# Optimization experiments

Measured on AMD Instinct MI355X. Metric: run time of the kernel, lower is better.

The kernel has to match this reference:

```python
import jax, jax.numpy as jnp
import numpy as np

ALPHA = 0.2  # LeakyReLU negative slope
NEG_INF = -9e15


def setup_inputs() -> dict:
    key = jax.random.key(0)
    k1, k2, k3, k4 = jax.random.split(key, 4)
    B, N, Fin, Fout = 4, 4096, 256, 128
    h = jax.random.normal(k1, (B, N, Fin), dtype=jnp.float32)
    adj = jax.random.randint(k2, (B, N, N), 0, 2, dtype=jnp.int32)  # {0,1} adjacency
    # xavier_uniform with gain 1.414
    limW = 1.414 * np.sqrt(6.0 / (Fin + Fout))
    W = jax.random.uniform(k3, (Fin, Fout), jnp.float32, -limW, limW)
    lima = 1.414 * np.sqrt(6.0 / (2 * Fout + 1))
    a = jax.random.uniform(k4, (2 * Fout, 1), jnp.float32, -lima, lima)
    return {"h": h, "adj": adj, "W": W, "a": a}


def reference(h, adj, W, a):
    # Wh: [B, N, Fout]
    Wh = jnp.einsum('bni,io->bno', h, W)
    Fout = W.shape[1]
    # Decompose a^T [Wh_i || Wh_j] = a1.Wh_i + a2.Wh_j (identical math, avoids
    # materializing the [B,N,N,2F] concat tensor the torch code builds).
    a1, a2 = a[:Fout, 0], a[Fout:, 0]
    s1 = jnp.einsum('bno,o->bn', Wh, a1)  # [B, N]
    s2 = jnp.einsum('bno,o->bn', Wh, a2)  # [B, N]
    e = jax.nn.leaky_relu(s1[:, :, None] + s2[:, None, :], negative_slope=ALPHA)  # [B,N,N]
    attention = jnp.where(adj > 0, e, jnp.asarray(NEG_INF, e.dtype))
    attention = jax.nn.softmax(attention, axis=2)
    # dropout is inactive in eval mode (training=False)
    # Faithful to the torch code: the FIRST h_prime is overwritten; the output is
    # einsum('bjk,bji->bki', attention, Wh) -> sums over the softmax (row) axis j.
    h_prime = jnp.einsum('bjk,bji->bki', attention, Wh)  # [B, N, Fout]
    return jax.nn.elu(h_prime)  # concat=True
```

## Files before the change

kernel.cpp:

```cpp
#include <hip/hip_runtime.h>
#include <hip/hip_bf16.h>

#define ALPHA 0.2f
#define L2E 1.4426950408889634f

constexpr int Nn = 4096;
constexpr int FIN = 256;
constexpr int FOUT = 128;
constexpr int JC = 4;
constexpr int JQ = 1024;
constexpr int NCH = 32;
constexpr long long SLAB = 2097152;

typedef __attribute__((ext_vector_type(8))) short short8;
typedef __attribute__((ext_vector_type(8))) unsigned short ushort8;
typedef __attribute__((ext_vector_type(4))) float f32x4;
typedef __attribute__((ext_vector_type(16))) float f32x16;
typedef __attribute__((ext_vector_type(4))) int int4v;

__device__ __forceinline__ unsigned short f2bf(float x) {
  unsigned int u = __float_as_uint(x);
  unsigned int r = (u + 0x7fffu + ((u >> 16) & 1u)) >> 16;
  return (unsigned short)r;
}

__device__ __forceinline__ float bf2f(unsigned short v) {
  return __uint_as_float(((unsigned)v) << 16);
}

__device__ __forceinline__ void gload16(const void* g, void* l) {
  auto lp = (__attribute__((address_space(3))) void*)l;
  auto gp = (const __attribute__((address_space(1))) void*)g;
  __builtin_amdgcn_global_load_lds(gp, lp, 16, 0, 0);
}

__global__ __launch_bounds__(256) void k0_prep(
    const float* __restrict__ W, unsigned short* __restrict__ WT) {
  __shared__ float lw[32][132];
  int t = threadIdx.x;
  int kc0 = blockIdx.x * 32;
#pragma unroll
  for (int m = 0; m < 4; ++m) {
    int idx = t * 16 + m * 4;
    f32x4 v = *(const f32x4*)(W + kc0 * 128 + idx);
    int k = idx >> 7, i0 = idx & 127;
    *(f32x4*)&lw[k][i0] = v;
  }
  __syncthreads();
  int i = t >> 1, half = t & 1;
  unsigned short pk[16];
#pragma unroll
  for (int kk = 0; kk < 16; ++kk) pk[kk] = f2bf(lw[half * 16 + kk][i]);
  ushort8* dst = (ushort8*)(WT + i * 256 + kc0 + half * 16);
  dst[0] = *(ushort8*)&pk[0];
  dst[1] = *(ushort8*)&pk[8];
}

__global__ __launch_bounds__(256) void k1b_wh(
    const float* __restrict__ h, const unsigned short* __restrict__ WT,
    const float* __restrict__ a, unsigned short* __restrict__ whT,
    float* __restrict__ s1L, float* __restrict__ s2L) {
  __shared__ __align__(16) char smem[36864];
  int t = threadIdx.x;
  int w = t >> 6, l = t & 63, g = l >> 4, r = l & 15;
  int r0 = blockIdx.x * 16;
  int b = r0 >> 12, nbase = r0 & 4095;

  f32x4 acc[2];
  acc[0] = (f32x4){0.f, 0.f, 0.f, 0.f};
  acc[1] = (f32x4){0.f, 0.f, 0.f, 0.f};

  for (int kc = 0; kc < 2; ++kc) {
    __syncthreads();
    {
      int row = t >> 4, sec = t & 15;
      const f32x4* src =
          (const f32x4*)(h + (long long)(r0 + row) * 256 + kc * 128 + sec * 8);
      f32x4 v0 = src[0], v1 = src[1];
      unsigned int pk[4];
      pk[0] = ((unsigned)f2bf(v0.y) << 16) | f2bf(v0.x);
      pk[1] = ((unsigned)f2bf(v0.w) << 16) | f2bf(v0.z);
      pk[2] = ((unsigned)f2bf(v1.y) << 16) | f2bf(v1.x);
      pk[3] = ((unsigned)f2bf(v1.w) << 16) | f2bf(v1.z);
      *(ushort8*)(smem + row * 256 + ((sec ^ (row & 7)) << 4)) = *(ushort8*)pk;
    }
    {
      int i = t >> 1, pt = t & 1;
      const ushort8* src = (const ushort8*)(WT + i * 256 + kc * 128 + pt * 64);
#pragma unroll
      for (int m = 0; m < 8; ++m) {
        ushort8 v = src[m];
        int slot = pt * 8 + m;
        *(ushort8*)(smem + 4096 + i * 256 + ((slot ^ (i & 7)) << 4)) = v;
      }
    }
    __syncthreads();
#pragma unroll
    for (int kk = 0; kk < 4; ++kk) {
      short8 af =
          *(const short8*)(smem + r * 256 + (((kk * 4 + g) ^ (r & 7)) << 4));
#pragma unroll
      for (int s = 0; s < 2; ++s) {
        int i = w * 32 + s * 16 + r;
        short8 bf = *(const short8*)(smem + 4096 + i * 256 +
                                     (((kk * 4 + g) ^ (i & 7)) << 4));
        acc[s] =
            __builtin_amdgcn_mfma_f32_16x16x32_bf16(af, bf, acc[s], 0, 0, 0);
      }
    }
  }

  __syncthreads();
  unsigned short* tb = (unsigned short*)smem;
#pragma unroll
  for (int s = 0; s < 2; ++s)
#pragma unroll
    for (int q = 0; q < 4; ++q)
      tb[(w * 32 + s * 16 + r) * 25 + g * 4 + q] = f2bf(acc[s][q]);
  __syncthreads();

  {
    int i = t >> 1, half = t & 1;
    ushort8 v = *(const ushort8*)(tb + i * 25 + half * 8);
    *(ushort8*)(whT + (((long long)(b * 128 + i)) << 12) + nbase + half * 8) =
        v;
  }
  {
    int n = t >> 4, seg = t & 15;
    f32x4 a10 = *(const f32x4*)(a + seg * 8);
    f32x4 a11 = *(const f32x4*)(a + seg * 8 + 4);
    f32x4 a20 = *(const f32x4*)(a + 128 + seg * 8);
    f32x4 a21 = *(const f32x4*)(a + 128 + seg * 8 + 4);
    float v1 = 0.f, v2 = 0.f;
#pragma unroll
    for (int m = 0; m < 8; ++m) {
      float wh = bf2f(tb[(seg * 8 + m) * 25 + n]);
      float c1 = (m < 4) ? a10[m] : a11[m - 4];
      float c2 = (m < 4) ? a20[m] : a21[m - 4];
      v1 += wh * c1;
      v2 += wh * c2;
    }
#pragma unroll
    for (int off = 8; off; off >>= 1) {
      v1 += __shfl_xor(v1, off);
      v2 += __shfl_xor(v2, off);
    }
    if (seg == 0) {
      s1L[r0 + n] = v1 * L2E;
      s2L[r0 + n] = v2 * L2E;
    }
  }
}

__global__ __launch_bounds__(256) void k2_stats(
    const int* __restrict__ adj, const float* __restrict__ s1L,
    const float* __restrict__ s2L, float2* __restrict__ st2,
    unsigned long long* __restrict__ mask64) {
  __shared__ unsigned int mwords[128];
  __shared__ float wsum[4];
  int row = blockIdx.x;
  int b = row >> 12;
  int t = threadIdx.x;
  float s1j = s1L[row];
  const int4v* arow = (const int4v*)(adj + (long long)row * Nn);
  const f32x4* s2v = (const f32x4*)(s2L + (b << 12));

  float sum = 0.f;
#pragma unroll
  for (int q = 0; q < 4; ++q) {
    int4v av = __builtin_nontemporal_load(arow + q * 256 + t);
    f32x4 sv = s2v[q * 256 + t];
    unsigned nib = 0;
#pragma unroll
    for (int c = 0; c < 4; ++c) {
      float u = s1j + sv[c];
      float vL = fmaxf(u, ALPHA * u);
      float e = exp2f(vL);
      sum += (av[c] > 0) ? e : 0.f;
      nib |= ((unsigned)(av[c] > 0)) << c;
    }
    unsigned n1 = nib | (__shfl_xor(nib, 1) << 4);
    unsigned n2 = n1 | (__shfl_xor(n1, 2) << 8);
    unsigned n4 = n2 | (__shfl_xor(n2, 4) << 16);
    if ((t & 7) == 0) mwords[q * 32 + (t >> 3)] = n4;
  }
#pragma unroll
  for (int off = 32; off; off >>= 1) sum += __shfl_xor(sum, off);
  if ((t & 63) == 0) wsum[t >> 6] = sum;
  __syncthreads();
  if (t < 64) {
    unsigned long long mv = *(unsigned long long*)&mwords[t * 2];
    mask64[((long long)row << 6) + t] = mv;
  }
  if (t == 0) {
    float S = wsum[0] + wsum[1] + wsum[2] + wsum[3];
    float negc = (S > 0.f) ? -log2f(S) : -1.0e30f;
    st2[row] = make_float2(s1j + negc, ALPHA * s1j + negc);
  }
}

__global__ __launch_bounds__(512, 4) void k3_pv(
    const unsigned short* __restrict__ whT, const float2* __restrict__ st2,
    const unsigned long long* __restrict__ mask64,
    const float* __restrict__ s2L, unsigned short* __restrict__ pbuf) {
  __shared__ __align__(16) char smem[40960];
  char* mbase = smem + 16384;
  float2* stl = (float2*)(smem + 32768);

  int t = threadIdx.x;
  int orig = blockIdx.x;
  int x = orig & 7, mm = orig >> 3;
  int b = x >> 1;
  int kt = ((x & 1) << 4) | (mm & 15);
  int jc = mm >> 4;
  int w = t >> 6, l = t & 63, hl = l >> 5, ln = l & 31;
  int ks = w & 3, jh = w >> 2;
  int jq0 = jc * JQ;
  long long brow = (long long)(b << 12);
  int k0 = kt << 7;
  float z1 = s2L[brow + k0 + ks * 32 + ln];
  float z2 = ALPHA * z1;
  int sh31 = 31 - ln;

  gload16(st2 + brow + jq0 + t * 2, (char*)stl + t * 16);
  {
    const char* m0 =
        (const char*)(mask64 + ((brow + jq0 + t) << 6)) + kt * 16;
    const char* m1 =
        (const char*)(mask64 + ((brow + jq0 + 512 + t) << 6)) + kt * 16;
    gload16(m0, mbase + t * 16);
    gload16(m1, mbase + 8192 + t * 16);
  }
  const unsigned short* whTb = whT + ((long long)b << 19);
  int joct0 = t >> 7, gi = t & 127;
  const unsigned short* wsrc0 =
      whTb + (long long)gi * 4096 + jq0 + joct0 * 8;
  gload16(wsrc0, smem + t * 16);
  __syncthreads();

  f32x16 acc[4];
#pragma unroll
  for (int q = 0; q < 4; ++q)
#pragma unroll
    for (int r = 0; r < 16; ++r) acc[q][r] = 0.f;

  for (int ch = 0; ch < NCH; ++ch) {
    int cur = ch & 1;
    if (ch + 1 < NCH)
      gload16(wsrc0 + (ch + 1) * 32, smem + (cur ^ 1) * 8192 + t * 16);
    char* wb = smem + cur * 8192;
    int jb = ch * 32 + jh * 16 + hl * 8;
    short8 af;
#pragma unroll
    for (int e = 0; e < 8; ++e) {
      int ja = jb + e;
      float2 sc = stl[ja];
      unsigned int mv = *(unsigned int*)(mbase + ja * 16 + ks * 4);
      float e1 = sc.x + z1;
      float e2 = sc.y + z2;
      float p = exp2f(fmaxf(e1, e2));
      int msk = ((int)(mv << sh31)) >> 31;
      unsigned pu = __float_as_uint(p) & (unsigned)msk;
      af[e] = (short)f2bf(__uint_as_float(pu));
    }
    int gb = (jh * 2 + hl) * 2048;
#pragma unroll
    for (int q = 0; q < 4; ++q) {
      short8 bv = *(const short8*)(wb + gb + ((q * 32 + ln) << 4));
      acc[q] = __builtin_amdgcn_mfma_f32_32x32x16_bf16(af, bv, acc[q], 0, 0, 0);
    }
    __syncthreads();
  }

  unsigned short* zone = (unsigned short*)smem;
  if (jh == 1) {
#pragma unroll
    for (int q = 0; q < 4; ++q)
#pragma unroll
      for (int r = 0; r < 16; ++r) {
        int kl = (r & 3) + ((r >> 2) << 3) + (hl << 2);
        zone[ks * 4096 + q * 1024 + kl * 32 + ln] = f2bf(acc[q][r]);
      }
  }
  __syncthreads();
  if (jh == 0) {
    unsigned short* pb = pbuf + (long long)jc * SLAB + ((brow + k0) << 7);
#pragma unroll
    for (int q = 0; q < 4; ++q)
#pragma unroll
      for (int r = 0; r < 16; ++r) {
        int kl = (r & 3) + ((r >> 2) << 3) + (hl << 2);
        float v = acc[q][r] + bf2f(zone[ks * 4096 + q * 1024 + kl * 32 + ln]);
        pb[(ks * 32 + kl) * 128 + q * 32 + ln] = f2bf(v);
      }
  }
}

__global__ __launch_bounds__(256) void k4_reduce(
    const unsigned short* __restrict__ pbuf, float* __restrict__ out) {
  int orig = blockIdx.x;
  int n = (orig & 7) * 128 + (orig >> 3);
  int base = (n * 256 + threadIdx.x) * 8;
  float s[8] = {0.f, 0.f, 0.f, 0.f, 0.f, 0.f, 0.f, 0.f};
#pragma unroll
  for (int sl = 0; sl < JC; ++sl) {
    ushort8 v = *(const ushort8*)(pbuf + (long long)sl * SLAB + base);
#pragma unroll
    for (int e = 0; e < 8; ++e)
      s[e] += __uint_as_float(((unsigned)(unsigned short)v[e]) << 16);
  }
  f32x4 o0, o1;
#pragma unroll
  for (int e = 0; e < 8; ++e) {
    float xv = s[e];
    float y = xv > 0.f ? xv : expm1f(xv);
    if (e < 4) o0[e] = y; else o1[e - 4] = y;
  }
  *(f32x4*)(out + base) = o0;
  *(f32x4*)(out + base + 4) = o1;
}

extern "C" void kernel_launch(void* const* d_in, const int* in_sizes, int n_in,
                              void* d_out, int out_size, void* d_ws,
                              size_t ws_size, hipStream_t stream) {
  const float* h = (const float*)d_in[0];
  const int* adj = (const int*)d_in[1];
  const float* W = (const float*)d_in[2];
  const float* a = (const float*)d_in[3];
  float* out = (float*)d_out;

  char* ws = (char*)d_ws;
  unsigned short* WT = (unsigned short*)ws;
  unsigned short* whT = (unsigned short*)(ws + (1 << 20));
  float* s1L = (float*)(ws + (5 << 20));
  float* s2L = s1L + 16384;
  float2* st2 = (float2*)(ws + (5 << 20) + (128 << 10));
  unsigned long long* mask64 =
      (unsigned long long*)(ws + (6 << 20));
  unsigned short* pbuf = (unsigned short*)(ws + (16 << 20));

  hipLaunchKernelGGL(k0_prep, dim3(8), dim3(256), 0, stream, W, WT);
  hipLaunchKernelGGL(k1b_wh, dim3(1024), dim3(256), 0, stream, h, WT, a, whT,
                     s1L, s2L);
  hipLaunchKernelGGL(k2_stats, dim3(16384), dim3(256), 0, stream, adj, s1L,
                     s2L, st2, mask64);
  hipLaunchKernelGGL(k3_pv, dim3(512), dim3(512), 0, stream, whT, st2, mask64,
                     s2L, pbuf);
  hipLaunchKernelGGL(k4_reduce, dim3(1024), dim3(256), 0, stream, pbuf, out);
}
```

Before: 123.6 us.

## Split PV kernel into more j-chunks using 16x16 MFMA tiles

The attention-times-Wh kernel now splits the j dimension into 8 chunks of 512 instead of 4 of 1024 and launches twice as many blocks. It switches from 32x32x16 to 16x16x32 bf16 MFMA tiles so each of the 8 waves owns 16 output rows, which removes the cross-wave reduction through shared memory. The mask words are stored in a transposed per-word plane layout, and the LDS footprint drops so more blocks can be resident. The stats kernel also replaces compare-and-select with an FMA on the 0/1 adjacency value. The cost is more partial slabs for the reduce kernel to sum, more redundant exp work per output, and a reliance on adjacency being exactly 0 or 1.

```diff
diff --git a/kernel.cpp b/kernel.cpp
--- a/kernel.cpp
+++ b/kernel.cpp
@@ -7,16 +7,16 @@
 constexpr int Nn = 4096;
 constexpr int FIN = 256;
 constexpr int FOUT = 128;
-constexpr int JC = 4;
-constexpr int JQ = 1024;
-constexpr int NCH = 32;
+constexpr int JC = 8;
+constexpr int JQ = 512;
+constexpr int NCH = 16;
 constexpr long long SLAB = 2097152;
 
 typedef __attribute__((ext_vector_type(8))) short short8;
 typedef __attribute__((ext_vector_type(8))) unsigned short ushort8;
 typedef __attribute__((ext_vector_type(4))) float f32x4;
-typedef __attribute__((ext_vector_type(16))) float f32x16;
 typedef __attribute__((ext_vector_type(4))) int int4v;
+typedef __attribute__((ext_vector_type(4))) unsigned int uint4v;
 
 __device__ __forceinline__ unsigned short f2bf(float x) {
   unsigned int u = __float_as_uint(x);
@@ -176,8 +176,8 @@
       float u = s1j + sv[c];
       float vL = fmaxf(u, ALPHA * u);
       float e = exp2f(vL);
-      sum += (av[c] > 0) ? e : 0.f;
-      nib |= ((unsigned)(av[c] > 0)) << c;
+      sum = fmaf((float)av[c], e, sum);
+      nib |= ((unsigned)av[c]) << c;
     }
     unsigned n1 = nib | (__shfl_xor(nib, 1) << 4);
     unsigned n2 = n1 | (__shfl_xor(n1, 2) << 8);
@@ -199,13 +199,13 @@
   }
 }
 
-__global__ __launch_bounds__(512, 4) void k3_pv(
+__global__ __launch_bounds__(512, 6) void k3_pv(
     const unsigned short* __restrict__ whT, const float2* __restrict__ st2,
     const unsigned long long* __restrict__ mask64,
     const float* __restrict__ s2L, unsigned short* __restrict__ pbuf) {
-  __shared__ __align__(16) char smem[40960];
-  char* mbase = smem + 16384;
-  float2* stl = (float2*)(smem + 32768);
+  __shared__ __align__(16) char smem[28672];
+  unsigned int* mkpl = (unsigned int*)(smem + 16384);
+  float2* stl = (float2*)(smem + 24576);
 
   int t = threadIdx.x;
   int orig = blockIdx.x;
@@ -213,86 +213,77 @@
   int b = x >> 1;
   int kt = ((x & 1) << 4) | (mm & 15);
   int jc = mm >> 4;
-  int w = t >> 6, l = t & 63, hl = l >> 5, ln = l & 31;
-  int ks = w & 3, jh = w >> 2;
+  int w = t >> 6, l = t & 63;
+  int lh = l >> 4;
+  int lo = l & 15;
+  int ks = w;
   int jq0 = jc * JQ;
   long long brow = (long long)(b << 12);
-  int k0 = kt << 7;
-  float z1 = s2L[brow + k0 + ks * 32 + ln];
+  int k0g = kt << 7;
+  float z1 = s2L[brow + k0g + ks * 16 + lo];
   float z2 = ALPHA * z1;
-  int sh31 = 31 - ln;
-
-  gload16(st2 + brow + jq0 + t * 2, (char*)stl + t * 16);
+  int sh31 = 31 - (((ks & 1) << 4) + lo);
+  int wsel = ks >> 1;
+
+  if (t < 256) gload16(st2 + brow + jq0 + t * 2, (char*)stl + t * 16);
   {
-    const char* m0 =
-        (const char*)(mask64 + ((brow + jq0 + t) << 6)) + kt * 16;
-    const char* m1 =
-        (const char*)(mask64 + ((brow + jq0 + 512 + t) << 6)) + kt * 16;
-    gload16(m0, mbase + t * 16);
-    gload16(m1, mbase + 8192 + t * 16);
+    uint4v mrow = *(const uint4v*)((const char*)(mask64 +
+                                                 ((brow + jq0 + t) << 6)) +
+                                   kt * 16);
+    mkpl[0 * 512 + t] = mrow[0];
+    mkpl[1 * 512 + t] = mrow[1];
+    mkpl[2 * 512 + t] = mrow[2];
+    mkpl[3 * 512 + t] = mrow[3];
   }
   const unsigned short* whTb = whT + ((long long)b << 19);
-  int joct0 = t >> 7, gi = t & 127;
+  int gi = t & 127;
   const unsigned short* wsrc0 =
-      whTb + (long long)gi * 4096 + jq0 + joct0 * 8;
+      whTb + (long long)gi * 4096 + jq0 + (t >> 7) * 8;
   gload16(wsrc0, smem + t * 16);
   __syncthreads();
 
-  f32x16 acc[4];
-#pragma unroll
-  for (int q = 0; q < 4; ++q)
-#pragma unroll
-    for (int r = 0; r < 16; ++r) acc[q][r] = 0.f;
-
+  f32x4 acc[8];
+#pragma unroll
+  for (int q = 0; q < 8; ++q) acc[q] = (f32x4){0.f, 0.f, 0.f, 0.f};
+
+  const unsigned int* mkw = mkpl + wsel * 512;
   for (int ch = 0; ch < NCH; ++ch) {
     int cur = ch & 1;
     if (ch + 1 < NCH)
       gload16(wsrc0 + (ch + 1) * 32, smem + (cur ^ 1) * 8192 + t * 16);
     char* wb = smem + cur * 8192;
-    int jb = ch * 32 + jh * 16 + hl * 8;
+    int jb = ch * 32 + lh * 8;
+    uint4v mw0 = *(const uint4v*)(mkw + jb);
+    uint4v mw1 = *(const uint4v*)(mkw + jb + 4);
     short8 af;
 #pragma unroll
     for (int e = 0; e < 8; ++e) {
-      int ja = jb + e;
-      float2 sc = stl[ja];
-      unsigned int mv = *(unsigned int*)(mbase + ja * 16 + ks * 4);
+      float2 sc = stl[jb + e];
+      unsigned mv = (e < 4) ? mw0[e] : mw1[e - 4];
       float e1 = sc.x + z1;
       float e2 = sc.y + z2;
       float p = exp2f(fmaxf(e1, e2));
       int msk = ((int)(mv << sh31)) >> 31;
       unsigned pu = __float_as_uint(p) & (unsigned)msk;
-      af[e] = (short)f2bf(__uint_as_float(pu));
-    }
-    int gb = (jh * 2 + hl) * 2048;
-#pragma unroll
-    for (int q = 0; q < 4; ++q) {
-      short8 bv = *(const short8*)(wb + gb + ((q * 32 + ln) << 4));
-      acc[q] = __builtin_amdgcn_mfma_f32_32x32x16_bf16(af, bv, acc[q], 0, 0, 0);
+      __hip_bfloat16 hb = __float2bfloat16(__uint_as_float(pu));
+      af[e] = *(short*)&hb;
+    }
+#pragma unroll
+    for (int q = 0; q < 8; ++q) {
+      short8 bv = *(const short8*)(wb + ((lh * 128 + q * 16 + lo) << 4));
+      acc[q] = __builtin_amdgcn_mfma_f32_16x16x32_bf16(af, bv, acc[q], 0, 0, 0);
     }
     __syncthreads();
   }
 
-  unsigned short* zone = (unsigned short*)smem;
-  if (jh == 1) {
-#pragma unroll
-    for (int q = 0; q < 4; ++q)
-#pragma unroll
-      for (int r = 0; r < 16; ++r) {
-        int kl = (r & 3) + ((r >> 2) << 3) + (hl << 2);
-        zone[ks * 4096 + q * 1024 + kl * 32 + ln] = f2bf(acc[q][r]);
-      }
-  }
-  __syncthreads();
-  if (jh == 0) {
-    unsigned short* pb = pbuf + (long long)jc * SLAB + ((brow + k0) << 7);
-#pragma unroll
-    for (int q = 0; q < 4; ++q)
-#pragma unroll
-      for (int r = 0; r < 16; ++r) {
-        int kl = (r & 3) + ((r >> 2) << 3) + (hl << 2);
-        float v = acc[q][r] + bf2f(zone[ks * 4096 + q * 1024 + kl * 32 + ln]);
-        pb[(ks * 32 + kl) * 128 + q * 32 + ln] = f2bf(v);
-      }
+  unsigned short* pb = pbuf + (long long)jc * SLAB + ((brow + k0g) << 7);
+#pragma unroll
+  for (int q = 0; q < 8; ++q) {
+#pragma unroll
+    for (int r = 0; r < 4; ++r) {
+      int kl = ks * 16 + lh * 4 + r;
+      pb[kl * 128 + q * 16 + lo] = f2bf(acc[q][r]);
+    }
   }
 }
 
@@ -344,7 +335,7 @@
                      s1L, s2L);
   hipLaunchKernelGGL(k2_stats, dim3(16384), dim3(256), 0, stream, adj, s1L,
                      s2L, st2, mask64);
-  hipLaunchKernelGGL(k3_pv, dim3(512), dim3(512), 0, stream, whT, st2, mask64,
-                     s2L, pbuf);
+  hipLaunchKernelGGL(k3_pv, dim3(1024), dim3(512), 0, stream, whT, st2,
+                     mask64, s2L, pbuf);
   hipLaunchKernelGGL(k4_reduce, dim3(1024), dim3(256), 0, stream, pbuf, out);
 }
```

After: 121.3 us. Within noise of the previous version (-1.8%).
